# Performance work log

Hardware: AMD Instinct MI355X
Metric: run time of the kernel (lower is better)

The kernel has to match this reference:

```python
import jax, jax.numpy as jnp
import numpy as np

K = 16384   # num_particles
IN = 512    # input_size
H = 1024    # hidden_size
ALPHA = 0.5 # resamp_alpha


def setup_inputs() -> dict:
    key = jax.random.key(0)
    ks = jax.random.split(key, 16)
    s = 0.02
    return {
        'input_': jax.random.normal(ks[0], (1, IN), jnp.float32),
        'h0': jax.random.uniform(ks[1], (K, H), jnp.float32),
        'p0': jax.random.normal(ks[2], (K, 1), jnp.float32),
        'eps': jax.random.normal(ks[3], (K, H), jnp.float32),
        'w_z': jax.random.normal(ks[4], (H + IN, H), jnp.float32) * s,
        'b_z': jnp.zeros((H,), jnp.float32),
        'w_r': jax.random.normal(ks[5], (H + IN, H), jnp.float32) * s,
        'b_r': jnp.zeros((H,), jnp.float32),
        'w_n': jax.random.normal(ks[6], (H + IN, 2 * H), jnp.float32) * s,
        'b_n': jnp.zeros((2 * H,), jnp.float32),
        'w_obs': jax.random.normal(ks[7], (H + IN, 1), jnp.float32) * s,
        'b_obs': jnp.zeros((1,), jnp.float32),
        'w_h1': jax.random.normal(ks[8], (H, 24), jnp.float32) * s,
        'b_h1': jnp.zeros((24,), jnp.float32),
        'w_h2': jax.random.normal(ks[9], (24, 2), jnp.float32) * s,
        'b_h2': jnp.zeros((2,), jnp.float32),
    }


def reference(input_, h0, p0, eps, w_z, b_z, w_r, b_r, w_n, b_n,
              w_obs, b_obs, w_h1, b_h1, w_h2, b_h2):
    # obs_in = input_.repeat(num_particles, 1)
    obs_in = jnp.broadcast_to(input_, (K, IN))          # [K, IN]
    obs_cat = jnp.concatenate([h0, obs_in], axis=1)     # [K, H+IN]
    z = jax.nn.sigmoid(obs_cat @ w_z + b_z)             # [K, H]
    r = jax.nn.sigmoid(obs_cat @ w_r + b_r)             # [K, H]
    n_pre = jnp.concatenate([r * h0, obs_in], axis=1) @ w_n + b_n  # [K, 2H]
    mu_n, var_n = n_pre[:, :H], n_pre[:, H:]
    # reparameterize: std = softplus(var), sample = mu + eps * std
    n = jnp.tanh(mu_n + eps * jax.nn.softplus(var_n))   # activation == 'tanh'
    h1 = (1.0 - z) * n + z * h0                         # [K, H]
    # observation likelihood -> normalized log weights over particles
    logpdf = jnp.concatenate([h1, obs_in], axis=1) @ w_obs + b_obs  # [K, 1]
    p1 = jax.nn.log_softmax(logpdf + p0, axis=0)        # [K, 1]
    # soft resampling (torch.multinomial with replacement)
    resamp_prob = ALPHA * jnp.exp(p1[:, 0]) + (1.0 - ALPHA) / K     # [K]
    idx = jax.random.categorical(jax.random.key(42), jnp.log(resamp_prob), shape=(K,))
    h1 = h1[idx]                                         # [K, H] gather
    pn = jnp.exp(p1[idx, 0])
    pn = pn / (ALPHA * pn + (1.0 - ALPHA) / K)
    pn = jnp.log(pn)
    p1 = (pn - jax.nn.logsumexp(pn, axis=0))[:, None]    # [K, 1]
    # exp-weighted reduce + small MLP head (dropout p=0 is identity)
    mean_hid = jnp.sum(jnp.exp(p1) * h1, axis=0)         # [H]
    loc_pred = jnp.maximum(mean_hid @ w_h1 + b_h1, 0.0) @ w_h2 + b_h2  # [2]
    return loc_pred, h1, p1
```

## Files before the change

### kernel.cpp

```cpp
#include <hip/hip_runtime.h>
#include <math.h>
#include <stdint.h>

#define KP 16384
#define IN_DIM 512
#define HD 1024
#define WQ 512
#define HOTCAP 1024

typedef _Float16 f16x8 __attribute__((ext_vector_type(8)));
typedef float f32x4 __attribute__((ext_vector_type(4)));

__device__ __forceinline__ uint32_t rotl(uint32_t x, uint32_t r) {
  return __builtin_amdgcn_alignbit(x, x, 32u - r);
}

__device__ __forceinline__ uint32_t tf_bits(uint32_t x1) {
  const uint32_t ks1 = 42u, ks2 = 42u ^ 0x1BD11BDAu;
  uint32_t x0 = x1;
  x1 = rotl(x1, 13) ^ x0;
  x0 += x1; x1 = rotl(x1, 15) ^ x0;
  x0 += x1; x1 = rotl(x1, 26) ^ x0;
  x0 += x1; x1 = rotl(x1, 6)  ^ x0;
  x0 += ks1; x1 += ks2 + 1u;
  x0 += x1; x1 = rotl(x1, 17) ^ x0;
  x0 += x1; x1 = rotl(x1, 29) ^ x0;
  x0 += x1; x1 = rotl(x1, 16) ^ x0;
  x0 += x1; x1 = rotl(x1, 24) ^ x0;
  x0 += ks2; x1 += 2u;
  x0 += x1; x1 = rotl(x1, 13) ^ x0;
  x0 += x1; x1 = rotl(x1, 15) ^ x0;
  x0 += x1; x1 = rotl(x1, 26) ^ x0;
  x0 += x1; x1 = rotl(x1, 6)  ^ x0;
  x1 += ks1 + 3u;
  x0 += x1; x1 = rotl(x1, 17) ^ x0;
  x0 += x1; x1 = rotl(x1, 29) ^ x0;
  x0 += x1; x1 = rotl(x1, 16) ^ x0;
  x0 += x1; x1 = rotl(x1, 24) ^ x0;
  x0 += ks1; x1 += ks2 + 4u;
  x0 += x1; x1 = rotl(x1, 13) ^ x0;
  x0 += x1; x1 = rotl(x1, 15) ^ x0;
  x0 += x1; x1 = rotl(x1, 26) ^ x0;
  x0 += x1; x1 = rotl(x1, 6)  ^ x0;
  x0 += ks2; x1 += 5u;
  return x0 ^ x1;
}

__device__ __forceinline__ float gumbel_from_bits(uint32_t b) {
  uint32_t ub = (b >> 9) | 0x3f800000u;
  float u = __uint_as_float(ub) - 1.0f;
  u = fmaxf(u, 1.1754943508222875e-38f);
  return -logf(-logf(u));
}

__device__ __forceinline__ unsigned long long pack_key(float g, int c) {
  uint32_t u = __float_as_uint(g);
  u = (u & 0x80000000u) ? ~u : (u | 0x80000000u);
  return ((unsigned long long)u << 32) | (uint32_t)(16383 - c);
}

__global__ __launch_bounds__(256) void bias_kernel(
    const float* __restrict__ in,
    const float* __restrict__ wz, const float* __restrict__ bz,
    const float* __restrict__ wr, const float* __restrict__ br,
    const float* __restrict__ wn, const float* __restrict__ bn,
    const float* __restrict__ wobs, const float* __restrict__ bobs,
    float* __restrict__ zb, float* __restrict__ rb,
    float* __restrict__ nb, float* __restrict__ ob) {
  __shared__ float sin_[IN_DIM];
  int t = threadIdx.x;
  for (int i = t; i < IN_DIM; i += 256) sin_[i] = in[i];
  __syncthreads();
  int gid = blockIdx.x * 256 + t;
  if (gid < 1024) {
    float s = bz[gid];
    for (int i = 0; i < IN_DIM; ++i) s = fmaf(sin_[i], wz[(HD + i) * HD + gid], s);
    zb[gid] = s;
  } else if (gid < 2048) {
    int j = gid - 1024;
    float s = br[j];
    for (int i = 0; i < IN_DIM; ++i) s = fmaf(sin_[i], wr[(HD + i) * HD + j], s);
    rb[j] = s;
  } else if (gid < 4096) {
    int j = gid - 2048;
    float s = bn[j];
    for (int i = 0; i < IN_DIM; ++i) s = fmaf(sin_[i], wn[(HD + i) * 2048 + j], s);
    nb[j] = s;
  } else if (gid == 4096) {
    float s = bobs[0];
    for (int i = 0; i < IN_DIM; ++i) s = fmaf(sin_[i], wobs[HD + i], s);
    ob[0] = s;
  }
}

__global__ __launch_bounds__(256) void splitw_kernel(
    const float* __restrict__ wz, const float* __restrict__ wr,
    const float* __restrict__ wn,
    _Float16* __restrict__ zHi, _Float16* __restrict__ zLo,
    _Float16* __restrict__ rHi, _Float16* __restrict__ rLo,
    _Float16* __restrict__ mHi, _Float16* __restrict__ mLo,
    _Float16* __restrict__ vHi, _Float16* __restrict__ vLo) {
  __shared__ float tile[32][33];
  int m = blockIdx.z;
  const float* src; int ld, cofs; _Float16 *oh, *ol;
  if (m == 0)      { src = wz; ld = 1024; cofs = 0;    oh = zHi; ol = zLo; }
  else if (m == 1) { src = wr; ld = 1024; cofs = 0;    oh = rHi; ol = rLo; }
  else if (m == 2) { src = wn; ld = 2048; cofs = 0;    oh = mHi; ol = mLo; }
  else             { src = wn; ld = 2048; cofs = 1024; oh = vHi; ol = vLo; }
  int k0 = blockIdx.x * 32, n0 = blockIdx.y * 32;
  int tx = threadIdx.x & 31, ty = threadIdx.x >> 5;
#pragma unroll
  for (int i = 0; i < 4; ++i) {
    int k = ty * 4 + i;
    tile[k][tx] = src[(size_t)(k0 + k) * ld + cofs + n0 + tx];
  }
  __syncthreads();
#pragma unroll
  for (int i = 0; i < 4; ++i) {
    int n = ty * 4 + i;
    float v = tile[tx][n] * 64.0f;
    _Float16 h = (_Float16)v;
    _Float16 l = (_Float16)((v - (float)h) * 2048.0f);
    oh[(size_t)(n0 + n) * 1024 + k0 + tx] = h;
    ol[(size_t)(n0 + n) * 1024 + k0 + tx] = l;
  }
}

#define LDH 40

__global__ __launch_bounds__(256, 2) void gemm_zr_mfma(
    const float* __restrict__ A,
    const _Float16* __restrict__ BzHi, const _Float16* __restrict__ BzLo,
    const _Float16* __restrict__ BrHi, const _Float16* __restrict__ BrLo,
    const float* __restrict__ zbias, const float* __restrict__ rbias,
    float* __restrict__ zout,
    _Float16* __restrict__ rhh, _Float16* __restrict__ rhl) {
  __shared__ __align__(16) _Float16 Ah[128 * LDH], Al[128 * LDH];
  __shared__ __align__(16) _Float16 B0h[64 * LDH], B0l[64 * LDH];
  __shared__ __align__(16) _Float16 B1h[64 * LDH], B1l[64 * LDH];
  int t = threadIdx.x;
  int row0 = blockIdx.x * 128, col0 = blockIdx.y * 64;
  int wave = t >> 6, lane = t & 63;
  int lr = lane & 15, hh = lane >> 4;
  int WR = (wave >> 1) * 64, WC = (wave & 1) * 32;

  f32x4 acc0[4][2][2] = {};
  f32x4 acc1[4][2][2] = {};

  for (int kb = 0; kb < 1024; kb += 32) {
#pragma unroll
    for (int p = 0; p < 2; ++p) {
      int id = t + p * 256;
      int row = id >> 2, kc = id & 3;
      const float* g = &A[(size_t)(row0 + row) * 1024 + kb + kc * 8];
      float4 v0 = *(const float4*)g;
      float4 v1 = *(const float4*)(g + 4);
      float vv[8] = {v0.x, v0.y, v0.z, v0.w, v1.x, v1.y, v1.z, v1.w};
      f16x8 hi, lo;
#pragma unroll
      for (int j = 0; j < 8; ++j) {
        _Float16 h = (_Float16)vv[j];
        hi[j] = h;
        lo[j] = (_Float16)((vv[j] - (float)h) * 2048.0f);
      }
      *(f16x8*)&Ah[row * LDH + kc * 8] = hi;
      *(f16x8*)&Al[row * LDH + kc * 8] = lo;
    }
    {
      int n = t >> 2, kc = t & 3;
      size_t gofs = (size_t)(col0 + n) * 1024 + kb + kc * 8;
      int lofs = n * LDH + kc * 8;
      *(f16x8*)&B0h[lofs] = *(const f16x8*)&BzHi[gofs];
      *(f16x8*)&B0l[lofs] = *(const f16x8*)&BzLo[gofs];
      *(f16x8*)&B1h[lofs] = *(const f16x8*)&BrHi[gofs];
      *(f16x8*)&B1l[lofs] = *(const f16x8*)&BrLo[gofs];
    }
    __syncthreads();
    f16x8 ah[4], al[4], bh[2][2], bl[2][2];
#pragma unroll
    for (int mt = 0; mt < 4; ++mt) {
      int r = WR + mt * 16 + lr;
      ah[mt] = *(f16x8*)&Ah[r * LDH + hh * 8];
      al[mt] = *(f16x8*)&Al[r * LDH + hh * 8];
    }
#pragma unroll
    for (int nt = 0; nt < 2; ++nt) {
      int c = WC + nt * 16 + lr;
      bh[0][nt] = *(f16x8*)&B0h[c * LDH + hh * 8];
      bl[0][nt] = *(f16x8*)&B0l[c * LDH + hh * 8];
      bh[1][nt] = *(f16x8*)&B1h[c * LDH + hh * 8];
      bl[1][nt] = *(f16x8*)&B1l[c * LDH + hh * 8];
    }
#pragma unroll
    for (int mt = 0; mt < 4; ++mt)
#pragma unroll
      for (int nt = 0; nt < 2; ++nt)
#pragma unroll
        for (int m = 0; m < 2; ++m) {
          acc0[mt][nt][m] = __builtin_amdgcn_mfma_f32_16x16x32_f16(ah[mt], bh[m][nt], acc0[mt][nt][m], 0, 0, 0);
          acc1[mt][nt][m] = __builtin_amdgcn_mfma_f32_16x16x32_f16(ah[mt], bl[m][nt], acc1[mt][nt][m], 0, 0, 0);
          acc1[mt][nt][m] = __builtin_amdgcn_mfma_f32_16x16x32_f16(al[mt], bh[m][nt], acc1[mt][nt][m], 0, 0, 0);
        }
    __syncthreads();
  }
  const float INV = 1.0f / 2048.0f, WS = 1.0f / 64.0f;
#pragma unroll
  for (int mt = 0; mt < 4; ++mt)
#pragma unroll
    for (int nt = 0; nt < 2; ++nt) {
      int col = col0 + WC + nt * 16 + lr;
#pragma unroll
      for (int q = 0; q < 4; ++q) {
        int row = row0 + WR + mt * 16 + hh * 4 + q;
        size_t off = (size_t)row * 1024 + col;
        float vz = (acc0[mt][nt][0][q] + acc1[mt][nt][0][q] * INV) * WS + zbias[col];
        float vr = (acc0[mt][nt][1][q] + acc1[mt][nt][1][q] * INV) * WS + rbias[col];
        float z = 1.0f / (1.0f + expf(-vz));
        float r = 1.0f / (1.0f + expf(-vr));
        float rv = r * A[off];
        zout[off] = z;
        _Float16 rhi = (_Float16)rv;
        rhh[off] = rhi;
        rhl[off] = (_Float16)((rv - (float)rhi) * 2048.0f);
      }
    }
}

__global__ __launch_bounds__(256, 2) void gemm_n_mfma(
    const _Float16* __restrict__ Ahg, const _Float16* __restrict__ Alg,
    const _Float16* __restrict__ BmHi, const _Float16* __restrict__ BmLo,
    const _Float16* __restrict__ BvHi, const _Float16* __restrict__ BvLo,
    const float* __restrict__ nbias,
    const float* __restrict__ h0, const float* __restrict__ eps,
    const float* __restrict__ zbuf, float* __restrict__ h1out) {
  __shared__ __align__(16) _Float16 Ah[128 * LDH], Al[128 * LDH];
  __shared__ __align__(16) _Float16 B0h[64 * LDH], B0l[64 * LDH];
  __shared__ __align__(16) _Float16 B1h[64 * LDH], B1l[64 * LDH];
  int t = threadIdx.x;
  int row0 = blockIdx.x * 128, col0 = blockIdx.y * 64;
  int wave = t >> 6, lane = t & 63;
  int lr = lane & 15, hh = lane >> 4;
  int WR = (wave >> 1) * 64, WC = (wave & 1) * 32;

  f32x4 acc0[4][2][2] = {};
  f32x4 acc1[4][2][2] = {};

  for (int kb = 0; kb < 1024; kb += 32) {
#pragma unroll
    for (int p = 0; p < 2; ++p) {
      int id = t + p * 256;
      int row = id >> 2, kc = id & 3;
      size_t g = (size_t)(row0 + row) * 1024 + kb + kc * 8;
      int lofs = row * LDH + kc * 8;
      *(f16x8*)&Ah[lofs] = *(const f16x8*)&Ahg[g];
      *(f16x8*)&Al[lofs] = *(const f16x8*)&Alg[g];
    }
    {
      int n = t >> 2, kc = t & 3;
      size_t gofs = (size_t)(col0 + n) * 1024 + kb + kc * 8;
      int lofs = n * LDH + kc * 8;
      *(f16x8*)&B0h[lofs] = *(const f16x8*)&BmHi[gofs];
      *(f16x8*)&B0l[lofs] = *(const f16x8*)&BmLo[gofs];
      *(f16x8*)&B1h[lofs] = *(const f16x8*)&BvHi[gofs];
      *(f16x8*)&B1l[lofs] = *(const f16x8*)&BvLo[gofs];
    }
    __syncthreads();
    f16x8 ah[4], al[4], bh[2][2], bl[2][2];
#pragma unroll
    for (int mt = 0; mt < 4; ++mt) {
      int r = WR + mt * 16 + lr;
      ah[mt] = *(f16x8*)&Ah[r * LDH + hh * 8];
      al[mt] = *(f16x8*)&Al[r * LDH + hh * 8];
    }
#pragma unroll
    for (int nt = 0; nt < 2; ++nt) {
      int c = WC + nt * 16 + lr;
      bh[0][nt] = *(f16x8*)&B0h[c * LDH + hh * 8];
      bl[0][nt] = *(f16x8*)&B0l[c * LDH + hh * 8];
      bh[1][nt] = *(f16x8*)&B1h[c * LDH + hh * 8];
      bl[1][nt] = *(f16x8*)&B1l[c * LDH + hh * 8];
    }
#pragma unroll
    for (int mt = 0; mt < 4; ++mt)
#pragma unroll
      for (int nt = 0; nt < 2; ++nt)
#pragma unroll
        for (int m = 0; m < 2; ++m) {
          acc0[mt][nt][m] = __builtin_amdgcn_mfma_f32_16x16x32_f16(ah[mt], bh[m][nt], acc0[mt][nt][m], 0, 0, 0);
          acc1[mt][nt][m] = __builtin_amdgcn_mfma_f32_16x16x32_f16(ah[mt], bl[m][nt], acc1[mt][nt][m], 0, 0, 0);
          acc1[mt][nt][m] = __builtin_amdgcn_mfma_f32_16x16x32_f16(al[mt], bh[m][nt], acc1[mt][nt][m], 0, 0, 0);
        }
    __syncthreads();
  }
  const float INV = 1.0f / 2048.0f, WS = 1.0f / 64.0f;
#pragma unroll
  for (int mt = 0; mt < 4; ++mt)
#pragma unroll
    for (int nt = 0; nt < 2; ++nt) {
      int col = col0 + WC + nt * 16 + lr;
#pragma unroll
      for (int q = 0; q < 4; ++q) {
        int row = row0 + WR + mt * 16 + hh * 4 + q;
        size_t off = (size_t)row * 1024 + col;
        float mu = (acc0[mt][nt][0][q] + acc1[mt][nt][0][q] * INV) * WS + nbias[col];
        float var = (acc0[mt][nt][1][q] + acc1[mt][nt][1][q] * INV) * WS + nbias[1024 + col];
        float sp = fmaxf(var, 0.0f) + log1pf(expf(-fabsf(var)));
        float n = tanhf(mu + eps[off] * sp);
        float z = zbuf[off];
        h1out[off] = (1.0f - z) * n + z * h0[off];
      }
    }
}

__global__ __launch_bounds__(256) void score_kernel(
    const float* __restrict__ h1, const float* __restrict__ wobs,
    const float* __restrict__ ob, const float* __restrict__ p0,
    float* __restrict__ s) {
  __shared__ float w[HD];
  int t = threadIdx.x;
  for (int i = t; i < HD; i += 256) w[i] = wobs[i];
  __syncthreads();
  int wave = t >> 6, lane = t & 63;
  int row = blockIdx.x * 4 + wave;
  float acc = 0.0f;
  for (int c = lane * 4; c < HD; c += 256) {
    float4 v = *(const float4*)&h1[(size_t)row * HD + c];
    acc = fmaf(v.x, w[c], acc);
    acc = fmaf(v.y, w[c + 1], acc);
    acc = fmaf(v.z, w[c + 2], acc);
    acc = fmaf(v.w, w[c + 3], acc);
  }
#pragma unroll
  for (int off = 32; off; off >>= 1) acc += __shfl_down(acc, off);
  if (lane == 0) s[row] = acc + ob[0] + p0[row];
}

__global__ __launch_bounds__(1024) void softmax_kernel(
    const float* __restrict__ s, float* __restrict__ p1v,
    float* __restrict__ logits, float* __restrict__ lmaxp,
    int* __restrict__ hotc, unsigned int* __restrict__ hotn) {
  __shared__ float red[1024];
  __shared__ int sc[1024];
  __shared__ float sh_thr;
  int t = threadIdx.x;
  float m = -INFINITY;
  for (int k = t; k < KP; k += 1024) m = fmaxf(m, s[k]);
  red[t] = m; __syncthreads();
  for (int o = 512; o; o >>= 1) { if (t < o) red[t] = fmaxf(red[t], red[t + o]); __syncthreads(); }
  m = red[0]; __syncthreads();
  float sum = 0.0f;
  for (int k = t; k < KP; k += 1024) sum += expf(s[k] - m);
  red[t] = sum; __syncthreads();
  for (int o = 512; o; o >>= 1) { if (t < o) red[t] += red[t + o]; __syncthreads(); }
  float ls = logf(red[0]);
  float lmax = logf(0.5f * expf(-ls) + (0.5f / KP));

  float lg[16];
#pragma unroll
  for (int j = 0; j < 16; ++j) {
    int k = t * 16 + j;
    float p = s[k] - m - ls;
    p1v[k] = p;
    lg[j] = logf(0.5f * expf(p) + (0.5f / KP));
    logits[k] = lg[j];
  }
  float chosen = INFINITY;
#pragma unroll
  for (int d = 2; d <= 10; d += 2) {
    float cand = lmax - (float)d;
    int cnt = 0;
#pragma unroll
    for (int j = 0; j < 16; ++j) cnt += (lg[j] > cand) ? 1 : 0;
    sc[t] = cnt; __syncthreads();
    for (int o = 512; o; o >>= 1) { if (t < o) sc[t] += sc[t + o]; __syncthreads(); }
    int total = sc[0]; __syncthreads();
    if (total <= HOTCAP) chosen = cand;
  }
  if (t == 0) sh_thr = chosen;
  __syncthreads();
  float hthr = sh_thr;
  int mycnt = 0;
#pragma unroll
  for (int j = 0; j < 16; ++j) mycnt += (lg[j] > hthr) ? 1 : 0;
  sc[t] = mycnt; __syncthreads();
  for (int o = 1; o < 1024; o <<= 1) {
    int v = (t >= o) ? sc[t - o] : 0;
    __syncthreads();
    sc[t] += v;
    __syncthreads();
  }
  int ofs = sc[t] - mycnt;
#pragma unroll
  for (int j = 0; j < 16; ++j) {
    if (lg[j] > hthr) hotc[ofs++] = t * 16 + j;
  }
  if (t == 1023) hotn[0] = (unsigned int)sc[1023];
  if (t == 0) lmaxp[0] = lmax;
}

__global__ __launch_bounds__(256) void thr_kernel(
    const float* __restrict__ logits, const float* __restrict__ lmaxp,
    const int* __restrict__ hotc, const unsigned int* __restrict__ hotn,
    uint32_t* __restrict__ sthr, unsigned long long* __restrict__ best) {
  int t = threadIdx.x;
  int wave = t >> 6, lane = t & 63;
  int r = blockIdx.x * 4 + wave;
  uint32_t base = ((uint32_t)r << 14) + 42u;

  unsigned long long key = 0ull;
#pragma unroll
  for (int j = 0; j < 4; ++j) {
    int c = lane + j * 64;
    uint32_t bits = tf_bits(base + (uint32_t)c);
    float g = gumbel_from_bits(bits) + logits[c];
    unsigned long long k2 = pack_key(g, c);
    if (k2 > key) key = k2;
  }
  int hn = (int)hotn[0];
  if (hn > HOTCAP) hn = HOTCAP;
  for (int i = lane; i < hn; i += 64) {
    int c = hotc[i];
    uint32_t bits = tf_bits(base + (uint32_t)c);
    float g = gumbel_from_bits(bits) + logits[c];
    unsigned long long k2 = pack_key(g, c);
    if (k2 > key) key = k2;
  }
#pragma unroll
  for (int off = 32; off; off >>= 1) {
    unsigned long long ok = __shfl_down(key, off);
    if (ok > key) key = ok;
  }
  if (lane == 0) {
    uint32_t u = (uint32_t)(key >> 32);
    u = (u & 0x80000000u) ? (u & 0x7FFFFFFFu) : ~u;
    float B0 = __uint_as_float(u);
    float wth = expf(lmaxp[0] + 1e-3f - B0);
    float omu = -expm1f(-wth);
    float delta = 8388608.0f * omu;
    uint32_t thr;
    if (delta >= 8388592.0f) thr = 0u;
    else {
      thr = 8388608u - (uint32_t)delta;
      thr = (thr > 24u) ? (thr - 24u) : 0u;
    }
    sthr[r] = thr << 9;
    best[r] = key;
  }
}

__global__ __launch_bounds__(256) void scan_kernel(
    const uint32_t* __restrict__ sthr, const float* __restrict__ logits,
    const unsigned long long* __restrict__ best, int* __restrict__ idx) {
  __shared__ uint32_t qb[4][WQ];
  __shared__ uint32_t qc[4][WQ];
  __shared__ unsigned long long redw[4];
  int t = threadIdx.x;
  int wave = t >> 6, lane = t & 63;
  unsigned long long lmask = (1ull << lane) - 1ull;

  for (int j = 0; j < 4; ++j) {
    int r = blockIdx.x * 4 + j;
    uint32_t thr = sthr[r];
    uint32_t base = ((uint32_t)r << 14) + 42u;
    unsigned long long mykey = 0ull;
    int wcnt = 0;
#pragma unroll 2
    for (int k = 0; k < 16; ++k) {
      uint32_t c0 = (uint32_t)k * 1024u + (uint32_t)t * 4u;
      uint32_t v0 = base + c0;
      uint32_t b0 = tf_bits(v0);
      uint32_t b1 = tf_bits(v0 + 1u);
      uint32_t b2 = tf_bits(v0 + 2u);
      uint32_t b3 = tf_bits(v0 + 3u);
#define QPUSH(bits, cc) {                                                 \
      bool pass = (bits) >= thr;                                          \
      unsigned long long mb = __ballot(pass);                             \
      if (mb) {                                                           \
        if (pass) {                                                       \
          int slot = wcnt + __popcll(mb & lmask);                         \
          if (slot < WQ) { qb[wave][slot] = (bits); qc[wave][slot] = (cc); } \
          else { float g = gumbel_from_bits(bits) + logits[cc];           \
                 unsigned long long kk = pack_key(g, (int)(cc));          \
                 if (kk > mykey) mykey = kk; }                            \
        }                                                                 \
        wcnt += __popcll(mb); } }
      QPUSH(b0, c0)
      QPUSH(b1, c0 + 1u)
      QPUSH(b2, c0 + 2u)
      QPUSH(b3, c0 + 3u)
#undef QPUSH
    }
    int n = wcnt < WQ ? wcnt : WQ;
    for (int i = lane; i < n; i += 64) {
      float g = gumbel_from_bits(qb[wave][i]) + logits[qc[wave][i]];
      unsigned long long kk = pack_key(g, (int)qc[wave][i]);
      if (kk > mykey) mykey = kk;
    }
#pragma unroll
    for (int off = 32; off; off >>= 1) {
      unsigned long long ok = __shfl_down(mykey, off);
      if (ok > mykey) mykey = ok;
    }
    if (lane == 0) redw[wave] = mykey;
    __syncthreads();
    if (t == 0) {
      unsigned long long k2 = best[r];
      for (int w = 0; w < 4; ++w) if (redw[w] > k2) k2 = redw[w];
      idx[r] = 16383 - (int)(k2 & 16383ull);
    }
    __syncthreads();
  }
}

__global__ __launch_bounds__(1024) void resample_kernel(
    const float* __restrict__ p1v, const int* __restrict__ idx,
    float* __restrict__ pn, float* __restrict__ p1out, float* __restrict__ wexp) {
  __shared__ float red[1024];
  int t = threadIdx.x;
  float m = -INFINITY;
  for (int k = t; k < KP; k += 1024) {
    float pv = p1v[idx[k]];
    float w = expf(pv);
    float v = logf(w / (0.5f * w + (0.5f / KP)));
    pn[k] = v;
    m = fmaxf(m, v);
  }
  red[t] = m; __syncthreads();
  for (int o = 512; o; o >>= 1) { if (t < o) red[t] = fmaxf(red[t], red[t + o]); __syncthreads(); }
  m = red[0]; __syncthreads();
  float sum = 0.0f;
  for (int k = t; k < KP; k += 1024) sum += expf(pn[k] - m);
  red[t] = sum; __syncthreads();
  for (int o = 512; o; o >>= 1) { if (t < o) red[t] += red[t + o]; __syncthreads(); }
  float lse = m + logf(red[0]);
  for (int k = t; k < KP; k += 1024) {
    float v = pn[k] - lse;
    p1out[k] = v;
    wexp[k] = expf(v);
  }
}

__global__ __launch_bounds__(256) void gather_kernel(
    const float* __restrict__ h1pre, const int* __restrict__ idx,
    const float* __restrict__ wexp, float* __restrict__ h1out,
    float* __restrict__ partials) {
  int t = threadIdx.x;
  int k0 = blockIdx.x * 64;
  float part[4] = {0.f, 0.f, 0.f, 0.f};
  for (int kk = 0; kk < 64; ++kk) {
    int k = k0 + kk;
    int src = idx[k];
    float w = wexp[k];
#pragma unroll
    for (int c = 0; c < 4; ++c) {
      float v = h1pre[(size_t)src * HD + t + c * 256];
      h1out[(size_t)k * HD + t + c * 256] = v;
      part[c] = fmaf(w, v, part[c]);
    }
  }
#pragma unroll
  for (int c = 0; c < 4; ++c) partials[(size_t)blockIdx.x * HD + t + c * 256] = part[c];
}

__global__ __launch_bounds__(256) void reduce_mean_kernel(
    const float* __restrict__ partials, float* __restrict__ mean_hid) {
  int j = blockIdx.x * 256 + threadIdx.x;
  float s = 0.0f;
  for (int b = 0; b < 256; ++b) s += partials[(size_t)b * HD + j];
  mean_hid[j] = s;
}

__global__ __launch_bounds__(64) void final_kernel(
    const float* __restrict__ mean_hid,
    const float* __restrict__ wh1, const float* __restrict__ bh1,
    const float* __restrict__ wh2, const float* __restrict__ bh2,
    float* __restrict__ out) {
  __shared__ float hrelu[24];
  int t = threadIdx.x;
  if (t < 24) {
    float s = bh1[t];
    for (int i = 0; i < HD; ++i) s = fmaf(mean_hid[i], wh1[i * 24 + t], s);
    hrelu[t] = fmaxf(s, 0.0f);
  }
  __syncthreads();
  if (t < 2) {
    float s = bh2[t];
    for (int j = 0; j < 24; ++j) s = fmaf(hrelu[j], wh2[j * 2 + t], s);
    out[t] = s;
  }
}

extern "C" void kernel_launch(void* const* d_in, const int* in_sizes, int n_in,
                              void* d_out, int out_size, void* d_ws, size_t ws_size,
                              hipStream_t stream) {
  (void)in_sizes; (void)n_in; (void)out_size; (void)ws_size;
  const float* input_ = (const float*)d_in[0];
  const float* h0    = (const float*)d_in[1];
  const float* p0    = (const float*)d_in[2];
  const float* eps   = (const float*)d_in[3];
  const float* w_z   = (const float*)d_in[4];
  const float* b_z   = (const float*)d_in[5];
  const float* w_r   = (const float*)d_in[6];
  const float* b_r   = (const float*)d_in[7];
  const float* w_n   = (const float*)d_in[8];
  const float* b_n   = (const float*)d_in[9];
  const float* w_obs = (const float*)d_in[10];
  const float* b_obs = (const float*)d_in[11];
  const float* w_h1  = (const float*)d_in[12];
  const float* b_h1  = (const float*)d_in[13];
  const float* w_h2  = (const float*)d_in[14];
  const float* b_h2  = (const float*)d_in[15];

  float* out = (float*)d_out;
  float* out_loc = out;
  float* out_h1  = out + 2;
  float* out_p1  = out + 2 + (size_t)KP * HD;

  _Float16* rhh  = (_Float16*)d_ws;
  _Float16* rhl  = rhh + (size_t)KP * HD;
  float* h1pre   = (float*)(rhl + (size_t)KP * HD);
  float* zb      = h1pre + (size_t)KP * HD;
  float* rb      = zb + 1024;
  float* nb      = rb + 1024;
  float* ob      = nb + 2048;
  float* sbuf    = ob + 16;
  float* p1v     = sbuf + KP;
  float* logits  = p1v + KP;
  float* pn      = logits + KP;
  float* wexpb   = pn + KP;
  float* mean_hid= wexpb + KP;
  float* partials= mean_hid + 1024;
  int*   idxb    = (int*)(partials + 256 * HD);
  uint32_t* sthrb = (uint32_t*)(idxb + KP);
  unsigned long long* bestb = (unsigned long long*)(sthrb + KP);
  int*   hotcb   = (int*)(bestb + KP);
  unsigned int* hotnb = (unsigned int*)(hotcb + HOTCAP);
  _Float16* wt   = (_Float16*)(hotnb + 16);
  _Float16* wzHi = wt;
  _Float16* wzLo = wt + 1 * (size_t)HD * HD;
  _Float16* wrHi = wt + 2 * (size_t)HD * HD;
  _Float16* wrLo = wt + 3 * (size_t)HD * HD;
  _Float16* wmHi = wt + 4 * (size_t)HD * HD;
  _Float16* wmLo = wt + 5 * (size_t)HD * HD;
  _Float16* wvHi = wt + 6 * (size_t)HD * HD;
  _Float16* wvLo = wt + 7 * (size_t)HD * HD;

  bias_kernel<<<17, 256, 0, stream>>>(input_, w_z, b_z, w_r, b_r, w_n, b_n,
                                      w_obs, b_obs, zb, rb, nb, ob);

  dim3 gs(32, 32, 4);
  splitw_kernel<<<gs, 256, 0, stream>>>(w_z, w_r, w_n, wzHi, wzLo, wrHi, wrLo,
                                        wmHi, wmLo, wvHi, wvLo);

  dim3 g1(KP / 128, HD / 64);
  gemm_zr_mfma<<<g1, 256, 0, stream>>>(h0, wzHi, wzLo, wrHi, wrLo, zb, rb,
                                       out_h1 , rhh, rhl);

  gemm_n_mfma<<<g1, 256, 0, stream>>>(rhh, rhl, wmHi, wmLo, wvHi, wvLo, nb,
                                      h0, eps, out_h1 , h1pre);

  score_kernel<<<KP / 4, 256, 0, stream>>>(h1pre, w_obs, ob, p0, sbuf);

  softmax_kernel<<<1, 1024, 0, stream>>>(sbuf, p1v, logits, ob + 8, hotcb, hotnb);

  thr_kernel<<<KP / 4, 256, 0, stream>>>(logits, ob + 8, hotcb, hotnb, sthrb, bestb);

  scan_kernel<<<4096, 256, 0, stream>>>(sthrb, logits, bestb, idxb);

  resample_kernel<<<1, 1024, 0, stream>>>(p1v, idxb, pn, out_p1, wexpb);

  gather_kernel<<<KP / 64, 256, 0, stream>>>(h1pre, idxb, wexpb, out_h1, partials);

  reduce_mean_kernel<<<4, 256, 0, stream>>>(partials, mean_hid);

  final_kernel<<<1, 64, 0, stream>>>(mean_hid, w_h1, b_h1, w_h2, b_h2, out_loc);
}
```

Baseline: 1.249 ms.

## Pre-split h0 into fp16 hi/lo once and add early-exit ballot in scan

Adds a standalone kernel that converts h0 into fp16 hi/lo halves once, stored in the h1pre workspace region. The z/r GEMM then loads these directly instead of reconverting fp32 tiles for each of its 16 column blocks, which cuts repeated fp32 reads and conversion ALU work. This costs an extra pass that writes 64MB. The scan kernel now takes a max over each 4-sample group and does one ballot to skip the per-sample ballots when no lane passes the threshold, and gets an occupancy hint of 6.

```diff
diff --git a/kernel.cpp b/kernel.cpp
--- a/kernel.cpp
+++ b/kernel.cpp
@@ -93,6 +93,24 @@
   }
 }
 
+__global__ __launch_bounds__(256) void splith_kernel(
+    const float* __restrict__ src, _Float16* __restrict__ hi,
+    _Float16* __restrict__ lo) {
+  size_t i = ((size_t)blockIdx.x * 256 + threadIdx.x) * 8;
+  float4 v0 = *(const float4*)&src[i];
+  float4 v1 = *(const float4*)&src[i + 4];
+  float vv[8] = {v0.x, v0.y, v0.z, v0.w, v1.x, v1.y, v1.z, v1.w};
+  f16x8 h8, l8;
+#pragma unroll
+  for (int j = 0; j < 8; ++j) {
+    _Float16 h = (_Float16)vv[j];
+    h8[j] = h;
+    l8[j] = (_Float16)((vv[j] - (float)h) * 2048.0f);
+  }
+  *(f16x8*)&hi[i] = h8;
+  *(f16x8*)&lo[i] = l8;
+}
+
 __global__ __launch_bounds__(256) void splitw_kernel(
     const float* __restrict__ wz, const float* __restrict__ wr,
     const float* __restrict__ wn,
@@ -130,6 +148,7 @@
 
 __global__ __launch_bounds__(256, 2) void gemm_zr_mfma(
     const float* __restrict__ A,
+    const _Float16* __restrict__ Ahg, const _Float16* __restrict__ Alg,
     const _Float16* __restrict__ BzHi, const _Float16* __restrict__ BzLo,
     const _Float16* __restrict__ BrHi, const _Float16* __restrict__ BrLo,
     const float* __restrict__ zbias, const float* __restrict__ rbias,
@@ -152,19 +171,10 @@
     for (int p = 0; p < 2; ++p) {
       int id = t + p * 256;
       int row = id >> 2, kc = id & 3;
-      const float* g = &A[(size_t)(row0 + row) * 1024 + kb + kc * 8];
-      float4 v0 = *(const float4*)g;
-      float4 v1 = *(const float4*)(g + 4);
-      float vv[8] = {v0.x, v0.y, v0.z, v0.w, v1.x, v1.y, v1.z, v1.w};
-      f16x8 hi, lo;
-#pragma unroll
-      for (int j = 0; j < 8; ++j) {
-        _Float16 h = (_Float16)vv[j];
-        hi[j] = h;
-        lo[j] = (_Float16)((vv[j] - (float)h) * 2048.0f);
-      }
-      *(f16x8*)&Ah[row * LDH + kc * 8] = hi;
-      *(f16x8*)&Al[row * LDH + kc * 8] = lo;
+      size_t g = (size_t)(row0 + row) * 1024 + kb + kc * 8;
+      int lofs = row * LDH + kc * 8;
+      *(f16x8*)&Ah[lofs] = *(const f16x8*)&Ahg[g];
+      *(f16x8*)&Al[lofs] = *(const f16x8*)&Alg[g];
     }
     {
       int n = t >> 2, kc = t & 3;
@@ -448,7 +458,7 @@
   }
 }
 
-__global__ __launch_bounds__(256) void scan_kernel(
+__global__ __launch_bounds__(256, 6) void scan_kernel(
     const uint32_t* __restrict__ sthr, const float* __restrict__ logits,
     const unsigned long long* __restrict__ best, int* __restrict__ idx) {
   __shared__ uint32_t qb[4][WQ];
@@ -472,23 +482,28 @@
       uint32_t b1 = tf_bits(v0 + 1u);
       uint32_t b2 = tf_bits(v0 + 2u);
       uint32_t b3 = tf_bits(v0 + 3u);
+      uint32_t m01 = b0 > b1 ? b0 : b1;
+      uint32_t m23 = b2 > b3 ? b2 : b3;
+      uint32_t mx = m01 > m23 ? m01 : m23;
+      if (__ballot(mx >= thr)) {
 #define QPUSH(bits, cc) {                                                 \
-      bool pass = (bits) >= thr;                                          \
-      unsigned long long mb = __ballot(pass);                             \
-      if (mb) {                                                           \
-        if (pass) {                                                       \
-          int slot = wcnt + __popcll(mb & lmask);                         \
-          if (slot < WQ) { qb[wave][slot] = (bits); qc[wave][slot] = (cc); } \
-          else { float g = gumbel_from_bits(bits) + logits[cc];           \
-                 unsigned long long kk = pack_key(g, (int)(cc));          \
-                 if (kk > mykey) mykey = kk; }                            \
-        }                                                                 \
-        wcnt += __popcll(mb); } }
-      QPUSH(b0, c0)
-      QPUSH(b1, c0 + 1u)
-      QPUSH(b2, c0 + 2u)
-      QPUSH(b3, c0 + 3u)
+        bool pass = (bits) >= thr;                                        \
+        unsigned long long mb = __ballot(pass);                           \
+        if (mb) {                                                         \
+          if (pass) {                                                     \
+            int slot = wcnt + __popcll(mb & lmask);                       \
+            if (slot < WQ) { qb[wave][slot] = (bits); qc[wave][slot] = (cc); } \
+            else { float g = gumbel_from_bits(bits) + logits[cc];         \
+                   unsigned long long kk = pack_key(g, (int)(cc));        \
+                   if (kk > mykey) mykey = kk; }                          \
+          }                                                               \
+          wcnt += __popcll(mb); } }
+        QPUSH(b0, c0)
+        QPUSH(b1, c0 + 1u)
+        QPUSH(b2, c0 + 2u)
+        QPUSH(b3, c0 + 3u)
 #undef QPUSH
+      }
     }
     int n = wcnt < WQ ? wcnt : WQ;
     for (int i = lane; i < n; i += 64) {
@@ -619,6 +634,8 @@
   _Float16* rhh  = (_Float16*)d_ws;
   _Float16* rhl  = rhh + (size_t)KP * HD;
   float* h1pre   = (float*)(rhl + (size_t)KP * HD);
+  _Float16* h0h  = (_Float16*)h1pre;
+  _Float16* h0l  = h0h + (size_t)KP * HD;
   float* zb      = h1pre + (size_t)KP * HD;
   float* rb      = zb + 1024;
   float* nb      = rb + 1024;
@@ -648,13 +665,15 @@
   bias_kernel<<<17, 256, 0, stream>>>(input_, w_z, b_z, w_r, b_r, w_n, b_n,
                                       w_obs, b_obs, zb, rb, nb, ob);
 
+  splith_kernel<<<KP * HD / 2048, 256, 0, stream>>>(h0, h0h, h0l);
+
   dim3 gs(32, 32, 4);
   splitw_kernel<<<gs, 256, 0, stream>>>(w_z, w_r, w_n, wzHi, wzLo, wrHi, wrLo,
                                         wmHi, wmLo, wvHi, wvLo);
 
   dim3 g1(KP / 128, HD / 64);
-  gemm_zr_mfma<<<g1, 256, 0, stream>>>(h0, wzHi, wzLo, wrHi, wrLo, zb, rb,
-                                       out_h1 , rhh, rhl);
+  gemm_zr_mfma<<<g1, 256, 0, stream>>>(h0, h0h, h0l, wzHi, wzLo, wrHi, wrLo,
+                                       zb, rb, out_h1 , rhh, rhl);
 
   gemm_n_mfma<<<g1, 256, 0, stream>>>(rhh, rhl, wmHi, wmLo, wvHi, wvLo, nb,
                                       h0, eps, out_h1 , h1pre);
```

Result: slower. 1.299 ms (+4.0%).

## Use direct global-to-LDS loads with XOR swizzle and pre-split h0 to fp16

Applied to the files above, without the earlier changes.

Both MFMA GEMMs now stage their A and B tiles with global_load_lds (a direct global-to-shared copy), which means the shared tiles use an unpadded 32-wide layout with an XOR swizzle to avoid bank conflicts. Because those loads cannot convert data on the way in, a new kernel splits h0 into fp16 hi/lo planes ahead of time, written into the h1pre workspace that is reused later. The gather kernel is reshaped to 1024-thread blocks handling 32 particles each, which doubles the number of partial sums that the reduce kernel must add. The gain is fewer VGPR staging steps and conversions inside the GEMM loop. The costs are an extra full read and write of h0 and the risk that the swizzle does not cover all bank conflicts.

```diff
diff --git a/kernel.cpp b/kernel.cpp
--- a/kernel.cpp
+++ b/kernel.cpp
@@ -10,6 +10,13 @@
 
 typedef _Float16 f16x8 __attribute__((ext_vector_type(8)));
 typedef float f32x4 __attribute__((ext_vector_type(4)));
+
+#define GLDS(g, l)                                                        \
+  __builtin_amdgcn_global_load_lds(                                       \
+      (const __attribute__((address_space(1))) void*)(g),                 \
+      (__attribute__((address_space(3))) void*)(l), 16, 0, 0)
+
+#define QSW(r) ((((r) & 3)) ^ (((r) >> 2) & 1))
 
 __device__ __forceinline__ uint32_t rotl(uint32_t x, uint32_t r) {
   return __builtin_amdgcn_alignbit(x, x, 32u - r);
@@ -93,6 +100,24 @@
   }
 }
 
+__global__ __launch_bounds__(256) void splith_kernel(
+    const float* __restrict__ src, _Float16* __restrict__ hi,
+    _Float16* __restrict__ lo) {
+  size_t i = ((size_t)blockIdx.x * 256 + threadIdx.x) * 8;
+  float4 v0 = *(const float4*)&src[i];
+  float4 v1 = *(const float4*)&src[i + 4];
+  float vv[8] = {v0.x, v0.y, v0.z, v0.w, v1.x, v1.y, v1.z, v1.w};
+  f16x8 h8, l8;
+#pragma unroll
+  for (int j = 0; j < 8; ++j) {
+    _Float16 h = (_Float16)vv[j];
+    h8[j] = h;
+    l8[j] = (_Float16)((vv[j] - (float)h) * 2048.0f);
+  }
+  *(f16x8*)&hi[i] = h8;
+  *(f16x8*)&lo[i] = l8;
+}
+
 __global__ __launch_bounds__(256) void splitw_kernel(
     const float* __restrict__ wz, const float* __restrict__ wr,
     const float* __restrict__ wn,
@@ -126,70 +151,61 @@
   }
 }
 
-#define LDH 40
-
 __global__ __launch_bounds__(256, 2) void gemm_zr_mfma(
     const float* __restrict__ A,
+    const _Float16* __restrict__ Ahg, const _Float16* __restrict__ Alg,
     const _Float16* __restrict__ BzHi, const _Float16* __restrict__ BzLo,
     const _Float16* __restrict__ BrHi, const _Float16* __restrict__ BrLo,
     const float* __restrict__ zbias, const float* __restrict__ rbias,
     float* __restrict__ zout,
     _Float16* __restrict__ rhh, _Float16* __restrict__ rhl) {
-  __shared__ __align__(16) _Float16 Ah[128 * LDH], Al[128 * LDH];
-  __shared__ __align__(16) _Float16 B0h[64 * LDH], B0l[64 * LDH];
-  __shared__ __align__(16) _Float16 B1h[64 * LDH], B1l[64 * LDH];
+  __shared__ __align__(16) _Float16 Ah[128 * 32], Al[128 * 32];
+  __shared__ __align__(16) _Float16 B0h[64 * 32], B0l[64 * 32];
+  __shared__ __align__(16) _Float16 B1h[64 * 32], B1l[64 * 32];
   int t = threadIdx.x;
   int row0 = blockIdx.x * 128, col0 = blockIdx.y * 64;
   int wave = t >> 6, lane = t & 63;
   int lr = lane & 15, hh = lane >> 4;
   int WR = (wave >> 1) * 64, WC = (wave & 1) * 32;
 
+  int arow0 = t >> 2,          akc0 = (t & 3) ^ QSW(arow0);
+  int arow1 = (t + 256) >> 2,  akc1 = (t & 3) ^ QSW(arow1);
+  int bn_   = t >> 2,          bkc  = (t & 3) ^ QSW(bn_);
+
   f32x4 acc0[4][2][2] = {};
   f32x4 acc1[4][2][2] = {};
 
   for (int kb = 0; kb < 1024; kb += 32) {
-#pragma unroll
-    for (int p = 0; p < 2; ++p) {
-      int id = t + p * 256;
-      int row = id >> 2, kc = id & 3;
-      const float* g = &A[(size_t)(row0 + row) * 1024 + kb + kc * 8];
-      float4 v0 = *(const float4*)g;
-      float4 v1 = *(const float4*)(g + 4);
-      float vv[8] = {v0.x, v0.y, v0.z, v0.w, v1.x, v1.y, v1.z, v1.w};
-      f16x8 hi, lo;
-#pragma unroll
-      for (int j = 0; j < 8; ++j) {
-        _Float16 h = (_Float16)vv[j];
-        hi[j] = h;
-        lo[j] = (_Float16)((vv[j] - (float)h) * 2048.0f);
-      }
-      *(f16x8*)&Ah[row * LDH + kc * 8] = hi;
-      *(f16x8*)&Al[row * LDH + kc * 8] = lo;
-    }
     {
-      int n = t >> 2, kc = t & 3;
-      size_t gofs = (size_t)(col0 + n) * 1024 + kb + kc * 8;
-      int lofs = n * LDH + kc * 8;
-      *(f16x8*)&B0h[lofs] = *(const f16x8*)&BzHi[gofs];
-      *(f16x8*)&B0l[lofs] = *(const f16x8*)&BzLo[gofs];
-      *(f16x8*)&B1h[lofs] = *(const f16x8*)&BrHi[gofs];
-      *(f16x8*)&B1l[lofs] = *(const f16x8*)&BrLo[gofs];
+      size_t g0 = (size_t)(row0 + arow0) * 1024 + kb + akc0 * 8;
+      size_t g1 = (size_t)(row0 + arow1) * 1024 + kb + akc1 * 8;
+      GLDS(&Ahg[g0], &Ah[t * 8]);
+      GLDS(&Alg[g0], &Al[t * 8]);
+      GLDS(&Ahg[g1], &Ah[(t + 256) * 8]);
+      GLDS(&Alg[g1], &Al[(t + 256) * 8]);
+      size_t gb = (size_t)(col0 + bn_) * 1024 + kb + bkc * 8;
+      GLDS(&BzHi[gb], &B0h[t * 8]);
+      GLDS(&BzLo[gb], &B0l[t * 8]);
+      GLDS(&BrHi[gb], &B1h[t * 8]);
+      GLDS(&BrLo[gb], &B1l[t * 8]);
     }
     __syncthreads();
     f16x8 ah[4], al[4], bh[2][2], bl[2][2];
 #pragma unroll
     for (int mt = 0; mt < 4; ++mt) {
       int r = WR + mt * 16 + lr;
-      ah[mt] = *(f16x8*)&Ah[r * LDH + hh * 8];
-      al[mt] = *(f16x8*)&Al[r * LDH + hh * 8];
+      int sa = hh ^ QSW(r);
+      ah[mt] = *(f16x8*)&Ah[r * 32 + sa * 8];
+      al[mt] = *(f16x8*)&Al[r * 32 + sa * 8];
     }
 #pragma unroll
     for (int nt = 0; nt < 2; ++nt) {
       int c = WC + nt * 16 + lr;
-      bh[0][nt] = *(f16x8*)&B0h[c * LDH + hh * 8];
-      bl[0][nt] = *(f16x8*)&B0l[c * LDH + hh * 8];
-      bh[1][nt] = *(f16x8*)&B1h[c * LDH + hh * 8];
-      bl[1][nt] = *(f16x8*)&B1l[c * LDH + hh * 8];
+      int sb = hh ^ QSW(c);
+      bh[0][nt] = *(f16x8*)&B0h[c * 32 + sb * 8];
+      bl[0][nt] = *(f16x8*)&B0l[c * 32 + sb * 8];
+      bh[1][nt] = *(f16x8*)&B1h[c * 32 + sb * 8];
+      bl[1][nt] = *(f16x8*)&B1l[c * 32 + sb * 8];
     }
 #pragma unroll
     for (int mt = 0; mt < 4; ++mt)
@@ -233,52 +249,53 @@
     const float* __restrict__ nbias,
     const float* __restrict__ h0, const float* __restrict__ eps,
     const float* __restrict__ zbuf, float* __restrict__ h1out) {
-  __shared__ __align__(16) _Float16 Ah[128 * LDH], Al[128 * LDH];
-  __shared__ __align__(16) _Float16 B0h[64 * LDH], B0l[64 * LDH];
-  __shared__ __align__(16) _Float16 B1h[64 * LDH], B1l[64 * LDH];
+  __shared__ __align__(16) _Float16 Ah[128 * 32], Al[128 * 32];
+  __shared__ __align__(16) _Float16 B0h[64 * 32], B0l[64 * 32];
+  __shared__ __align__(16) _Float16 B1h[64 * 32], B1l[64 * 32];
   int t = threadIdx.x;
   int row0 = blockIdx.x * 128, col0 = blockIdx.y * 64;
   int wave = t >> 6, lane = t & 63;
   int lr = lane & 15, hh = lane >> 4;
   int WR = (wave >> 1) * 64, WC = (wave & 1) * 32;
 
+  int arow0 = t >> 2,          akc0 = (t & 3) ^ QSW(arow0);
+  int arow1 = (t + 256) >> 2,  akc1 = (t & 3) ^ QSW(arow1);
+  int bn_   = t >> 2,          bkc  = (t & 3) ^ QSW(bn_);
+
   f32x4 acc0[4][2][2] = {};
   f32x4 acc1[4][2][2] = {};
 
   for (int kb = 0; kb < 1024; kb += 32) {
-#pragma unroll
-    for (int p = 0; p < 2; ++p) {
-      int id = t + p * 256;
-      int row = id >> 2, kc = id & 3;
-      size_t g = (size_t)(row0 + row) * 1024 + kb + kc * 8;
-      int lofs = row * LDH + kc * 8;
-      *(f16x8*)&Ah[lofs] = *(const f16x8*)&Ahg[g];
-      *(f16x8*)&Al[lofs] = *(const f16x8*)&Alg[g];
-    }
     {
-      int n = t >> 2, kc = t & 3;
-      size_t gofs = (size_t)(col0 + n) * 1024 + kb + kc * 8;
-      int lofs = n * LDH + kc * 8;
-      *(f16x8*)&B0h[lofs] = *(const f16x8*)&BmHi[gofs];
-      *(f16x8*)&B0l[lofs] = *(const f16x8*)&BmLo[gofs];
-      *(f16x8*)&B1h[lofs] = *(const f16x8*)&BvHi[gofs];
-      *(f16x8*)&B1l[lofs] = *(const f16x8*)&BvLo[gofs];
+      size_t g0 = (size_t)(row0 + arow0) * 1024 + kb + akc0 * 8;
+      size_t g1 = (size_t)(row0 + arow1) * 1024 + kb + akc1 * 8;
+      GLDS(&Ahg[g0], &Ah[t * 8]);
+      GLDS(&Alg[g0], &Al[t * 8]);
+      GLDS(&Ahg[g1], &Ah[(t + 256) * 8]);
+      GLDS(&Alg[g1], &Al[(t + 256) * 8]);
+      size_t gb = (size_t)(col0 + bn_) * 1024 + kb + bkc * 8;
+      GLDS(&BmHi[gb], &B0h[t * 8]);
+      GLDS(&BmLo[gb], &B0l[t * 8]);
+      GLDS(&BvHi[gb], &B1h[t * 8]);
+      GLDS(&BvLo[gb], &B1l[t * 8]);
     }
     __syncthreads();
     f16x8 ah[4], al[4], bh[2][2], bl[2][2];
 #pragma unroll
     for (int mt = 0; mt < 4; ++mt) {
       int r = WR + mt * 16 + lr;
-      ah[mt] = *(f16x8*)&Ah[r * LDH + hh * 8];
-      al[mt] = *(f16x8*)&Al[r * LDH + hh * 8];
+      int sa = hh ^ QSW(r);
+      ah[mt] = *(f16x8*)&Ah[r * 32 + sa * 8];
+      al[mt] = *(f16x8*)&Al[r * 32 + sa * 8];
     }
 #pragma unroll
     for (int nt = 0; nt < 2; ++nt) {
       int c = WC + nt * 16 + lr;
-      bh[0][nt] = *(f16x8*)&B0h[c * LDH + hh * 8];
-      bl[0][nt] = *(f16x8*)&B0l[c * LDH + hh * 8];
-      bh[1][nt] = *(f16x8*)&B1h[c * LDH + hh * 8];
-      bl[1][nt] = *(f16x8*)&B1l[c * LDH + hh * 8];
+      int sb = hh ^ QSW(c);
+      bh[0][nt] = *(f16x8*)&B0h[c * 32 + sb * 8];
+      bl[0][nt] = *(f16x8*)&B0l[c * 32 + sb * 8];
+      bh[1][nt] = *(f16x8*)&B1h[c * 32 + sb * 8];
+      bl[1][nt] = *(f16x8*)&B1l[c * 32 + sb * 8];
     }
 #pragma unroll
     for (int mt = 0; mt < 4; ++mt)
@@ -540,33 +557,29 @@
   }
 }
 
-__global__ __launch_bounds__(256) void gather_kernel(
+__global__ __launch_bounds__(1024) void gather_kernel(
     const float* __restrict__ h1pre, const int* __restrict__ idx,
     const float* __restrict__ wexp, float* __restrict__ h1out,
     float* __restrict__ partials) {
   int t = threadIdx.x;
-  int k0 = blockIdx.x * 64;
-  float part[4] = {0.f, 0.f, 0.f, 0.f};
-  for (int kk = 0; kk < 64; ++kk) {
+  int k0 = blockIdx.x * 32;
+  float part = 0.0f;
+  for (int kk = 0; kk < 32; ++kk) {
     int k = k0 + kk;
     int src = idx[k];
     float w = wexp[k];
-#pragma unroll
-    for (int c = 0; c < 4; ++c) {
-      float v = h1pre[(size_t)src * HD + t + c * 256];
-      h1out[(size_t)k * HD + t + c * 256] = v;
-      part[c] = fmaf(w, v, part[c]);
-    }
-  }
-#pragma unroll
-  for (int c = 0; c < 4; ++c) partials[(size_t)blockIdx.x * HD + t + c * 256] = part[c];
+    float v = h1pre[(size_t)src * HD + t];
+    h1out[(size_t)k * HD + t] = v;
+    part = fmaf(w, v, part);
+  }
+  partials[(size_t)blockIdx.x * HD + t] = part;
 }
 
 __global__ __launch_bounds__(256) void reduce_mean_kernel(
     const float* __restrict__ partials, float* __restrict__ mean_hid) {
   int j = blockIdx.x * 256 + threadIdx.x;
   float s = 0.0f;
-  for (int b = 0; b < 256; ++b) s += partials[(size_t)b * HD + j];
+  for (int b = 0; b < 512; ++b) s += partials[(size_t)b * HD + j];
   mean_hid[j] = s;
 }
 
@@ -619,6 +632,8 @@
   _Float16* rhh  = (_Float16*)d_ws;
   _Float16* rhl  = rhh + (size_t)KP * HD;
   float* h1pre   = (float*)(rhl + (size_t)KP * HD);
+  _Float16* h0h  = (_Float16*)h1pre;
+  _Float16* h0l  = h0h + (size_t)KP * HD;
   float* zb      = h1pre + (size_t)KP * HD;
   float* rb      = zb + 1024;
   float* nb      = rb + 1024;
@@ -630,7 +645,7 @@
   float* wexpb   = pn + KP;
   float* mean_hid= wexpb + KP;
   float* partials= mean_hid + 1024;
-  int*   idxb    = (int*)(partials + 256 * HD);
+  int*   idxb    = (int*)(partials + 512 * HD);
   uint32_t* sthrb = (uint32_t*)(idxb + KP);
   unsigned long long* bestb = (unsigned long long*)(sthrb + KP);
   int*   hotcb   = (int*)(bestb + KP);
@@ -648,13 +663,15 @@
   bias_kernel<<<17, 256, 0, stream>>>(input_, w_z, b_z, w_r, b_r, w_n, b_n,
                                       w_obs, b_obs, zb, rb, nb, ob);
 
+  splith_kernel<<<KP * HD / 2048, 256, 0, stream>>>(h0, h0h, h0l);
+
   dim3 gs(32, 32, 4);
   splitw_kernel<<<gs, 256, 0, stream>>>(w_z, w_r, w_n, wzHi, wzLo, wrHi, wrLo,
                                         wmHi, wmLo, wvHi, wvLo);
 
   dim3 g1(KP / 128, HD / 64);
-  gemm_zr_mfma<<<g1, 256, 0, stream>>>(h0, wzHi, wzLo, wrHi, wrLo, zb, rb,
-                                       out_h1 , rhh, rhl);
+  gemm_zr_mfma<<<g1, 256, 0, stream>>>(h0, h0h, h0l, wzHi, wzLo, wrHi, wrLo,
+                                       zb, rb, out_h1 , rhh, rhl);
 
   gemm_n_mfma<<<g1, 256, 0, stream>>>(rhh, rhl, wmHi, wmLo, wvHi, wvLo, nb,
                                       h0, eps, out_h1 , h1pre);
@@ -669,7 +686,7 @@
 
   resample_kernel<<<1, 1024, 0, stream>>>(p1v, idxb, pn, out_p1, wexpb);
 
-  gather_kernel<<<KP / 64, 256, 0, stream>>>(h1pre, idxb, wexpb, out_h1, partials);
+  gather_kernel<<<512, 1024, 0, stream>>>(h1pre, idxb, wexpb, out_h1, partials);
 
   reduce_mean_kernel<<<4, 256, 0, stream>>>(partials, mean_hid);
 
```

Result: slower. 1.304 ms (+4.4%).
